# Optimization experiments

Measured on AMD Instinct MI355X. Metric: run time of the kernel, lower is better.

Reference implementation:

```python
import jax, jax.numpy as jnp
import numpy as np

N_REL = 8
N_LAYERS = 2


def setup_inputs() -> dict:
    key = jax.random.key(0)
    ks = jax.random.split(key, 8)
    N, E, D = 32768, 524288, 384
    x = jax.random.normal(ks[0], (N, D), jnp.float32)
    edge_index = jax.random.randint(ks[1], (2, E), 0, N, dtype=jnp.int32)
    edge_type = jax.random.randint(ks[2], (E,), 0, N_REL, dtype=jnp.int32)
    W_rel = jax.random.normal(ks[3], (N_REL, D, D), jnp.float32) * 0.05
    b_rel = jnp.zeros((N_REL, D), jnp.float32)
    norm_constants = jnp.ones((N_REL,), jnp.float32)
    W_mp = jax.random.normal(ks[4], (D, D), jnp.float32) * 0.05
    b_mp = jnp.zeros((D,), jnp.float32)
    W_self = jax.random.normal(ks[5], (D, D), jnp.float32) * 0.05
    b_self = jnp.zeros((D,), jnp.float32)
    return {"x": x, "edge_index": edge_index, "edge_type": edge_type,
            "batch_size": 128, "W_rel": W_rel, "b_rel": b_rel,
            "norm_constants": norm_constants, "W_mp": W_mp, "b_mp": b_mp,
            "W_self": W_self, "b_self": b_self}


def reference(x, edge_index, edge_type, batch_size, W_rel, b_rel,
              norm_constants, W_mp, b_mp, W_self, b_self):
    N = x.shape[0]
    src, dst = edge_index[0], edge_index[1]  # PyG: row0=source j, row1=target i
    # per-edge cosine similarity == pairwise_cosine_similarity(x)[dst, src]
    x_n = x / jnp.linalg.norm(x, axis=1, keepdims=True)
    cos_e = jnp.sum(x_n[dst] * x_n[src], axis=-1)  # [E]
    h = x
    for _ in range(N_LAYERS):
        # ---- RelationAwareMP: per-relation gather-linear-scale-scatter ----
        out = jnp.zeros((N, W_rel.shape[-1]), h.dtype)
        for r in range(N_REL):
            w = jnp.where(edge_type == r, cos_e / norm_constants[r], 0.0)  # [E]
            lin_h = h @ W_rel[r] + b_rel[r]           # [N, D] (linear commutes w/ gather)
            msg = w[:, None] * lin_h[src]             # [E, D]
            out = out + jax.ops.segment_sum(msg, dst, num_segments=N)
        h = jax.nn.relu(out)
        # ---- MP: add-aggregated linear messages + self transform ----
        lin_h = h @ W_mp + b_mp                       # [N, D]
        agg = jax.ops.segment_sum(lin_h[src], dst, num_segments=N)
        h = jax.nn.relu(agg + (h @ W_self + b_self))
    # [N, D] -> [B, N/B, D] -> mean over nodes per graph
    h = h.reshape(batch_size, -1, h.shape[-1])
    return h.mean(axis=1)
```

## Files before the change

kernel.cpp:

```cpp
#include <hip/hip_runtime.h>
#include <stdint.h>

typedef unsigned short u16;
typedef unsigned int u32;
typedef __attribute__((ext_vector_type(4))) float f32x4;
typedef __attribute__((ext_vector_type(8))) short bf16x8;

#define NN 32768
#define EE 524288
#define DD 384
#define NREL 8
#define NGR 128
#define NCAT (NREL * DD)

__device__ __forceinline__ float bf2f(u16 u) {
  union { u32 u; float f; } v; v.u = ((u32)u) << 16; return v.f;
}
__device__ __forceinline__ u16 f2bf(float f) {
  union { float f; u32 u; } v; v.f = f;
  u32 r = v.u + 0x7fffu + ((v.u >> 16) & 1u);
  return (u16)(r >> 16);
}
__device__ __forceinline__ float2 up2(u32 p) {
  return make_float2(bf2f((u16)(p & 0xffffu)), bf2f((u16)(p >> 16)));
}
__device__ __forceinline__ u32 pk2(float a, float b) {
  return (u32)f2bf(a) | ((u32)f2bf(b) << 16);
}
__device__ __forceinline__ void gl16(const u16* g, char* s) {
  __builtin_amdgcn_global_load_lds(
      (const __attribute__((address_space(1))) unsigned int*)(const void*)g,
      (__attribute__((address_space(3))) unsigned int*)(void*)s, 16, 0, 0);
}
__device__ __forceinline__ float dot4(uint4 a, uint4 b) {
  float2 p, q; float acc;
  p = up2(a.x); q = up2(b.x); acc  = p.x * q.x + p.y * q.y;
  p = up2(a.y); q = up2(b.y); acc += p.x * q.x + p.y * q.y;
  p = up2(a.z); q = up2(b.z); acc += p.x * q.x + p.y * q.y;
  p = up2(a.w); q = up2(b.w); acc += p.x * q.x + p.y * q.y;
  return acc;
}

__global__ __launch_bounds__(256) void k_invnorm(const float* __restrict__ x,
                                                 float* __restrict__ invn,
                                                 u16* __restrict__ h0,
                                                 int* __restrict__ cur) {
  const int gid = blockIdx.x * 256 + threadIdx.x;
  if (gid < NN) cur[gid] = 0;
  const int node = gid >> 6;
  const int l = threadIdx.x & 63;
  const float* row = x + (size_t)node * DD;
  float v[6];
  float s = 0.f;
#pragma unroll
  for (int j = 0; j < 6; ++j) { v[j] = row[l + 64 * j]; s += v[j] * v[j]; }
#pragma unroll
  for (int off = 32; off > 0; off >>= 1) s += __shfl_xor(s, off, 64);
  if (l == 0) invn[node] = rsqrtf(s);
  u16* hr = h0 + (size_t)node * DD;
#pragma unroll
  for (int j = 0; j < 6; ++j) hr[l + 64 * j] = f2bf(v[j]);
}

__global__ void k_prepW(const float* __restrict__ Wrel, const float* __restrict__ Wmp,
                        const float* __restrict__ Wself,
                        u16* __restrict__ W3T, u16* __restrict__ W2T) {
  const int i = blockIdx.x * 256 + threadIdx.x;
  const int total1 = NCAT * DD;
  const int total2 = DD * 768;
  if (i < total1) {
    const int ncat = i / DD, k = i % DD;
    const int r = ncat / DD, n = ncat % DD;
    W3T[i] = f2bf(Wrel[(size_t)r * DD * DD + (size_t)k * DD + n]);
  } else if (i < total1 + total2) {
    const int ii = i - total1;
    const int j = ii / 768, k = ii % 768;
    const float v = (k < DD) ? Wmp[k * DD + j] : Wself[(k - DD) * DD + j];
    W2T[ii] = f2bf(v);
  }
}

__global__ __launch_bounds__(256) void k_cos(const u16* __restrict__ H,
                                             const float* __restrict__ invn,
                                             const int* __restrict__ ei,
                                             const int* __restrict__ ety,
                                             const float* __restrict__ ncs,
                                             float* __restrict__ we,
                                             int* __restrict__ cnt) {
  const int e = (int)((blockIdx.x * 256 + threadIdx.x) >> 4);
  const int sub = threadIdx.x & 15;
  const int s = ei[e], d = ei[EE + e];
  const uint4* rs = (const uint4*)(H + (size_t)s * DD);
  const uint4* rd = (const uint4*)(H + (size_t)d * DD);
  float acc = 0.f;
#pragma unroll
  for (int j = 0; j < 3; ++j) acc += dot4(rs[sub + 16 * j], rd[sub + 16 * j]);
#pragma unroll
  for (int m = 1; m < 16; m <<= 1) acc += __shfl_xor(acc, m, 64);
  if (sub == 0) {
    we[e] = acc * invn[s] * invn[d] / ncs[ety[e]];
    atomicAdd(&cnt[d], 1);
  }
}

__global__ __launch_bounds__(1024) void k_scan(const int* __restrict__ deg,
                                               int* __restrict__ rp,
                                               int* __restrict__ cur) {
  __shared__ int ps[1024];
  const int t = threadIdx.x;
  const int base = t * 32;
  int loc[32];
  int tot = 0;
#pragma unroll
  for (int j = 0; j < 32; ++j) { loc[j] = tot; tot += deg[base + j]; }
  ps[t] = tot;
  __syncthreads();
  for (int off = 1; off < 1024; off <<= 1) {
    const int v = (t >= off) ? ps[t - off] : 0;
    __syncthreads();
    ps[t] += v;
    __syncthreads();
  }
  const int myoff = ps[t] - tot;
#pragma unroll
  for (int j = 0; j < 32; ++j) {
    const int val = myoff + loc[j];
    rp[base + j] = val;
    cur[base + j] = val;
  }
  if (t == 1023) rp[NN] = EE;
}

__global__ void k_scatter(const int* __restrict__ ei, const int* __restrict__ etype,
                          const float* __restrict__ we, int* __restrict__ cur,
                          int* __restrict__ epack, float* __restrict__ wsort) {
  const int e = blockIdx.x * 256 + threadIdx.x;
  const int d = ei[EE + e];
  const int pos = atomicAdd(&cur[d], 1);
  epack[pos] = ei[e] | (etype[e] << 16);
  wsort[pos] = we[e];
}

__global__ __launch_bounds__(256) void k_gemm_lin(
    const u16* __restrict__ A, const u16* __restrict__ Bt,
    u16* __restrict__ lin) {
  constexpr int K = DD;
  constexpr int NT = 24;
  __shared__ __align__(16) u16 As[128 * 64];
  __shared__ __align__(16) u16 Bs[128 * 64];
  const int tid = threadIdx.x;
  const int w = tid >> 6, l = tid & 63;
  const int per = gridDim.x >> 3;
  const int rpx = per / NT;
  const int xcd = blockIdx.x & 7;
  const int idx = blockIdx.x >> 3;
  const int mb = (xcd * rpx + idx / NT) * 128;
  const int nb = (idx % NT) * 128;
  const int wr = (w >> 1) * 64;
  const int wc = (w & 1) * 64;
  const int sr = tid >> 3;
  const int swz16 = ((l & 7) ^ (l >> 3)) * 8;
  const int lr = l & 15;
  const int cb = l >> 4;
  const int sx = l & 7;
  char* asb = (char*)As;
  char* bsb = (char*)Bs;
  const int wb = w * 1024;
  f32x4 acc[4][4] = {};
  const u16* a0 = A + (size_t)(mb + sr) * K + swz16;
  const u16* b0 = Bt + (size_t)(nb + sr) * K + swz16;
  const size_t r32 = (size_t)32 * K;
  for (int k0 = 0; k0 < K; k0 += 64) {
    gl16(a0 + k0,           asb + wb);
    gl16(a0 + k0 + r32,     asb + wb + 4096);
    gl16(a0 + k0 + 2 * r32, asb + wb + 8192);
    gl16(a0 + k0 + 3 * r32, asb + wb + 12288);
    gl16(b0 + k0,           bsb + wb);
    gl16(b0 + k0 + r32,     bsb + wb + 4096);
    gl16(b0 + k0 + 2 * r32, bsb + wb + 8192);
    gl16(b0 + k0 + 3 * r32, bsb + wb + 12288);
    __syncthreads();
#pragma unroll
    for (int kk = 0; kk < 64; kk += 32) {
      const int cs = (((kk >> 3) + cb) ^ sx) << 4;
      bf16x8 af[4], bfr[4];
#pragma unroll
      for (int m = 0; m < 4; ++m)
        af[m] = *(const bf16x8*)((const char*)As + (wr + m * 16 + lr) * 128 + cs);
#pragma unroll
      for (int n = 0; n < 4; ++n)
        bfr[n] = *(const bf16x8*)((const char*)Bs + (wc + n * 16 + lr) * 128 + cs);
#pragma unroll
      for (int m = 0; m < 4; ++m)
#pragma unroll
        for (int n = 0; n < 4; ++n)
          acc[m][n] = __builtin_amdgcn_mfma_f32_16x16x32_bf16(af[m], bfr[n], acc[m][n], 0, 0, 0);
    }
    __syncthreads();
  }
  const int lg = l >> 4;
#pragma unroll
  for (int n = 0; n < 4; ++n) {
    const int col = nb + wc + n * 16 + lr;
#pragma unroll
    for (int m = 0; m < 4; ++m) {
#pragma unroll
      for (int q = 0; q < 4; ++q) {
        const int row = mb + wr + m * 16 + lg * 4 + q;
        lin[(size_t)row * NCAT + col] = f2bf(acc[m][n][q]);
      }
    }
  }
}

#define EL_BODY(PK, W)                                                        \
  {                                                                           \
    const int src_ = (PK) & 0xffff;                                           \
    const int ty_ = (PK) >> 16;                                               \
    const u32* r_ = (const u32*)(lin + (size_t)src_ * NCAT + ty_ * DD) + 3 * l; \
    const u32 x0_ = r_[0], x1_ = r_[1], x2_ = r_[2];                          \
    float2 p_;                                                                \
    p_ = up2(x0_); a0 += (W) * p_.x; a1 += (W) * p_.y;                        \
    p_ = up2(x1_); a2 += (W) * p_.x; a3 += (W) * p_.y;                        \
    p_ = up2(x2_); a4 += (W) * p_.x; a5 += (W) * p_.y;                        \
    switch (ty_) {                                                            \
      case 0: s0 += (W); break; case 1: s1 += (W); break;                     \
      case 2: s2 += (W); break; case 3: s3 += (W); break;                     \
      case 4: s4 += (W); break; case 5: s5 += (W); break;                     \
      case 6: s6 += (W); break; default: s7 += (W); break;                    \
    }                                                                         \
  }

__global__ __launch_bounds__(256) void k_edge_lin(
    const u16* __restrict__ lin, const int* __restrict__ rp,
    const int* __restrict__ epack, const float* __restrict__ wsort,
    const float* __restrict__ brel, u16* __restrict__ H2) {
  const int i = blockIdx.x * 4 + (threadIdx.x >> 6);
  const int l = threadIdx.x & 63;
  const int e0 = rp[i], e1 = rp[i + 1];
  float a0 = 0, a1 = 0, a2 = 0, a3 = 0, a4 = 0, a5 = 0;
  float s0 = 0, s1 = 0, s2 = 0, s3 = 0, s4 = 0, s5 = 0, s6 = 0, s7 = 0;
  int e = e0;
  for (; e + 4 <= e1; e += 4) {
    const int pkA = epack[e], pkB = epack[e + 1], pkC = epack[e + 2], pkD = epack[e + 3];
    const float wA = wsort[e], wB = wsort[e + 1], wC = wsort[e + 2], wD = wsort[e + 3];
    EL_BODY(pkA, wA)
    EL_BODY(pkB, wB)
    EL_BODY(pkC, wC)
    EL_BODY(pkD, wD)
  }
  for (; e < e1; ++e) {
    const int pk = epack[e];
    const float w = wsort[e];
    EL_BODY(pk, w)
  }
  const float* bp = brel + 6 * l;
  float b0 = 0, b1 = 0, b2 = 0, b3 = 0, b4 = 0, b5 = 0;
#pragma unroll
  for (int r = 0; r < 8; ++r) {
    const float sr = (r == 0) ? s0 : (r == 1) ? s1 : (r == 2) ? s2 : (r == 3) ? s3
                   : (r == 4) ? s4 : (r == 5) ? s5 : (r == 6) ? s6 : s7;
    const float* bq = bp + r * DD;
    b0 += sr * bq[0]; b1 += sr * bq[1]; b2 += sr * bq[2];
    b3 += sr * bq[3]; b4 += sr * bq[4]; b5 += sr * bq[5];
  }
  u32* o = (u32*)(H2 + (size_t)i * DD + 6 * l);
  o[0] = pk2(fmaxf(a0 + b0, 0.f), fmaxf(a1 + b1, 0.f));
  o[1] = pk2(fmaxf(a2 + b2, 0.f), fmaxf(a3 + b3, 0.f));
  o[2] = pk2(fmaxf(a4 + b4, 0.f), fmaxf(a5 + b5, 0.f));
}

#define ES_BODY(SRC)                                                          \
  {                                                                           \
    const u32* r_ = (const u32*)(H2 + (size_t)(SRC) * DD) + 3 * l;            \
    const u32 x0_ = r_[0], x1_ = r_[1], x2_ = r_[2];                          \
    float2 p_;                                                                \
    p_ = up2(x0_); a0 += p_.x; a1 += p_.y;                                    \
    p_ = up2(x1_); a2 += p_.x; a3 += p_.y;                                    \
    p_ = up2(x2_); a4 += p_.x; a5 += p_.y;                                    \
  }

__global__ __launch_bounds__(256) void k_edge_sum(
    const u16* __restrict__ H2, const int* __restrict__ rp,
    const int* __restrict__ epack, u16* __restrict__ smp) {
  const int i = blockIdx.x * 4 + (threadIdx.x >> 6);
  const int l = threadIdx.x & 63;
  const int e0 = rp[i], e1 = rp[i + 1];
  float a0 = 0, a1 = 0, a2 = 0, a3 = 0, a4 = 0, a5 = 0;
  int e = e0;
  for (; e + 4 <= e1; e += 4) {
    const int sA = epack[e] & 0xffff, sB = epack[e + 1] & 0xffff;
    const int sC = epack[e + 2] & 0xffff, sD = epack[e + 3] & 0xffff;
    ES_BODY(sA) ES_BODY(sB) ES_BODY(sC) ES_BODY(sD)
  }
  for (; e < e1; ++e) {
    const int s = epack[e] & 0xffff;
    ES_BODY(s)
  }
  u32* o = (u32*)(smp + (size_t)i * DD + 6 * l);
  o[0] = pk2(a0, a1);
  o[1] = pk2(a2, a3);
  o[2] = pk2(a4, a5);
}

__global__ __launch_bounds__(256) void k_gemm_mp(
    const u16* __restrict__ A0, const u16* __restrict__ A1,
    const u16* __restrict__ Bt, u16* __restrict__ o_bf,
    const float* __restrict__ bmp, const float* __restrict__ bself,
    const int* __restrict__ rp) {
  constexpr int K = 768;
  constexpr int AS = DD;
  constexpr int NT = 3;
  __shared__ __align__(16) u16 As[128 * 64];
  __shared__ __align__(16) u16 Bs[128 * 64];
  const int tid = threadIdx.x;
  const int w = tid >> 6, l = tid & 63;
  const int per = gridDim.x >> 3;
  const int rpx = per / NT;
  const int xcd = blockIdx.x & 7;
  const int idx = blockIdx.x >> 3;
  const int mb = (xcd * rpx + idx / NT) * 128;
  const int nb = (idx % NT) * 128;
  const int wr = (w >> 1) * 64;
  const int wc = (w & 1) * 64;
  const int sr = tid >> 3;
  const int swz16 = ((l & 7) ^ (l >> 3)) * 8;
  const int lr = l & 15;
  const int cb = l >> 4;
  const int sx = l & 7;
  char* asb = (char*)As;
  char* bsb = (char*)Bs;
  const int wb = w * 1024;
  f32x4 acc[4][4] = {};
  const u16* b0 = Bt + (size_t)(nb + sr) * K + swz16;
  const size_t br32 = (size_t)32 * K;
  const size_t ar32 = (size_t)32 * AS;
  for (int k0 = 0; k0 < K; k0 += 64) {
    const u16* Ab; int ak;
    if (k0 >= DD) { Ab = A1; ak = k0 - DD; }
    else { Ab = A0; ak = k0; }
    const u16* ap = Ab + (size_t)(mb + sr) * AS + ak + swz16;
    gl16(ap,            asb + wb);
    gl16(ap + ar32,     asb + wb + 4096);
    gl16(ap + 2 * ar32, asb + wb + 8192);
    gl16(ap + 3 * ar32, asb + wb + 12288);
    gl16(b0 + k0,            bsb + wb);
    gl16(b0 + k0 + br32,     bsb + wb + 4096);
    gl16(b0 + k0 + 2 * br32, bsb + wb + 8192);
    gl16(b0 + k0 + 3 * br32, bsb + wb + 12288);
    __syncthreads();
#pragma unroll
    for (int kk = 0; kk < 64; kk += 32) {
      const int cs = (((kk >> 3) + cb) ^ sx) << 4;
      bf16x8 af[4], bfr[4];
#pragma unroll
      for (int m = 0; m < 4; ++m)
        af[m] = *(const bf16x8*)((const char*)As + (wr + m * 16 + lr) * 128 + cs);
#pragma unroll
      for (int n = 0; n < 4; ++n)
        bfr[n] = *(const bf16x8*)((const char*)Bs + (wc + n * 16 + lr) * 128 + cs);
#pragma unroll
      for (int m = 0; m < 4; ++m)
#pragma unroll
        for (int n = 0; n < 4; ++n)
          acc[m][n] = __builtin_amdgcn_mfma_f32_16x16x32_bf16(af[m], bfr[n], acc[m][n], 0, 0, 0);
    }
    __syncthreads();
  }
  const int lg = l >> 4;
#pragma unroll
  for (int n = 0; n < 4; ++n) {
    const int col = nb + wc + n * 16 + lr;
    const float bb = bmp[col];
    const float bs = bself[col];
#pragma unroll
    for (int m = 0; m < 4; ++m) {
#pragma unroll
      for (int q = 0; q < 4; ++q) {
        const int row = mb + wr + m * 16 + lg * 4 + q;
        float v = acc[m][n][q];
        const float deg = (float)(rp[row + 1] - rp[row]);
        v = fmaxf(v + deg * bb + bs, 0.f);
        o_bf[(size_t)row * DD + col] = f2bf(v);
      }
    }
  }
}

__global__ __launch_bounds__(192) void k_mean(const u16* __restrict__ H,
                                              float* __restrict__ out) {
  const int g = blockIdx.x, t = threadIdx.x;
  float ax = 0.f, ay = 0.f;
  const u16* base = H + (size_t)g * 256 * DD;
  for (int j = 0; j < 256; ++j) {
    const float2 hv = up2(*(const u32*)(base + (size_t)j * DD + 2 * t));
    ax += hv.x; ay += hv.y;
  }
  out[g * DD + 2 * t]     = ax * (1.f / 256.f);
  out[g * DD + 2 * t + 1] = ay * (1.f / 256.f);
}

extern "C" void kernel_launch(void* const* d_in, const int* in_sizes, int n_in,
                              void* d_out, int out_size, void* d_ws, size_t ws_size,
                              hipStream_t stream) {
  const float* x     = (const float*)d_in[0];
  const int*   ei    = (const int*)d_in[1];
  const int*   ety   = (const int*)d_in[2];
  const float* Wrel  = (const float*)d_in[4];
  const float* brel  = (const float*)d_in[5];
  const float* ncs   = (const float*)d_in[6];
  const float* Wmp   = (const float*)d_in[7];
  const float* bmp   = (const float*)d_in[8];
  const float* Wself = (const float*)d_in[9];
  const float* bself = (const float*)d_in[10];
  float* out = (float*)d_out;
  (void)in_sizes; (void)n_in; (void)out_size; (void)ws_size;

  char* ws = (char*)d_ws;
  size_t off = 0;
  auto alloc = [&](size_t bytes) {
    void* p = ws + off;
    off = (off + bytes + 255) & ~(size_t)255;
    return p;
  };
  float* invn  = (float*)alloc((size_t)NN * 4);
  int*   rp    = (int*)alloc(((size_t)NN + 1) * 4);
  int*   cur   = (int*)alloc((size_t)NN * 4);
  float* we    = (float*)alloc((size_t)EE * 4);
  int*   epack = (int*)alloc((size_t)EE * 4);
  float* wsort = (float*)alloc((size_t)EE * 4);
  u16*   W3T   = (u16*)alloc((size_t)NCAT * DD * 2);
  u16*   W2T   = (u16*)alloc((size_t)DD * 768 * 2);
  u16*   H     = (u16*)alloc((size_t)NN * DD * 2);
  u16*   H2    = (u16*)alloc((size_t)NN * DD * 2);
  u16*   lin   = (u16*)alloc((size_t)NN * NCAT * 2);
  u16*   smp   = lin;

  k_invnorm<<<NN / 4, 256, 0, stream>>>(x, invn, H, cur);
  k_prepW<<<(NCAT * DD + DD * 768 + 255) / 256, 256, 0, stream>>>(Wrel, Wmp, Wself, W3T, W2T);
  k_cos<<<EE / 16, 256, 0, stream>>>(H, invn, ei, ety, ncs, we, cur);
  k_scan<<<1, 1024, 0, stream>>>(cur, rp, cur);
  k_scatter<<<EE / 256, 256, 0, stream>>>(ei, ety, we, cur, epack, wsort);

  for (int layer = 0; layer < 2; ++layer) {
    k_gemm_lin<<<24 * NN / 128, 256, 0, stream>>>(H, W3T, lin);
    k_edge_lin<<<NN / 4, 256, 0, stream>>>(lin, rp, epack, wsort, brel, H2);
    k_edge_sum<<<NN / 4, 256, 0, stream>>>(H2, rp, epack, smp);
    k_gemm_mp<<<3 * NN / 128, 256, 0, stream>>>(smp, H2, W2T, H, bmp, bself, rp);
  }
  k_mean<<<NGR, 192, 0, stream>>>(H, out);
}
```

Measured before the change: 702.8 us.

## Split relation GEMM and edge gather into two halves of four relations

The per-relation linear output (N x 8D bf16, about 200MB) is now computed in two halves of four relations, each followed by an edge-gather pass. The smaller 100MB buffer is meant to fit better in cache (MI355X has a large last-level cache), so the random gathers hit cache more often. The cost is an extra fp32 partial-sum buffer that is written and read back, two more kernel launches, and edge lists that are now scanned twice.

```diff
diff --git a/kernel.cpp b/kernel.cpp
--- a/kernel.cpp
+++ b/kernel.cpp
@@ -12,6 +12,7 @@
 #define NREL 8
 #define NGR 128
 #define NCAT (NREL * DD)
+#define LHALF 1536
 
 __device__ __forceinline__ float bf2f(u16 u) {
   union { u32 u; float f; } v; v.u = ((u32)u) << 16; return v.f;
@@ -142,10 +143,10 @@
 }
 
 __global__ __launch_bounds__(256) void k_gemm_lin(
-    const u16* __restrict__ A, const u16* __restrict__ Bt,
+    const u16* __restrict__ A, const u16* __restrict__ BtH,
     u16* __restrict__ lin) {
   constexpr int K = DD;
-  constexpr int NT = 24;
+  constexpr int NT = 12;
   __shared__ __align__(16) u16 As[128 * 64];
   __shared__ __align__(16) u16 Bs[128 * 64];
   const int tid = threadIdx.x;
@@ -168,7 +169,7 @@
   const int wb = w * 1024;
   f32x4 acc[4][4] = {};
   const u16* a0 = A + (size_t)(mb + sr) * K + swz16;
-  const u16* b0 = Bt + (size_t)(nb + sr) * K + swz16;
+  const u16* b0 = BtH + (size_t)(nb + sr) * K + swz16;
   const size_t r32 = (size_t)32 * K;
   for (int k0 = 0; k0 < K; k0 += 64) {
     gl16(a0 + k0,           asb + wb);
@@ -207,67 +208,80 @@
 #pragma unroll
       for (int q = 0; q < 4; ++q) {
         const int row = mb + wr + m * 16 + lg * 4 + q;
-        lin[(size_t)row * NCAT + col] = f2bf(acc[m][n][q]);
+        lin[(size_t)row * LHALF + col] = f2bf(acc[m][n][q]);
       }
     }
   }
 }
 
-#define EL_BODY(PK, W)                                                        \
+#define EH_BODY(PK, W)                                                        \
   {                                                                           \
-    const int src_ = (PK) & 0xffff;                                           \
     const int ty_ = (PK) >> 16;                                               \
-    const u32* r_ = (const u32*)(lin + (size_t)src_ * NCAT + ty_ * DD) + 3 * l; \
-    const u32 x0_ = r_[0], x1_ = r_[1], x2_ = r_[2];                          \
-    float2 p_;                                                                \
-    p_ = up2(x0_); a0 += (W) * p_.x; a1 += (W) * p_.y;                        \
-    p_ = up2(x1_); a2 += (W) * p_.x; a3 += (W) * p_.y;                        \
-    p_ = up2(x2_); a4 += (W) * p_.x; a5 += (W) * p_.y;                        \
-    switch (ty_) {                                                            \
-      case 0: s0 += (W); break; case 1: s1 += (W); break;                     \
-      case 2: s2 += (W); break; case 3: s3 += (W); break;                     \
-      case 4: s4 += (W); break; case 5: s5 += (W); break;                     \
-      case 6: s6 += (W); break; default: s7 += (W); break;                    \
+    if (PASS == 0 ? (ty_ < 4) : (ty_ >= 4)) {                                 \
+      const int tl_ = PASS == 0 ? ty_ : ty_ - 4;                              \
+      const int src_ = (PK) & 0xffff;                                         \
+      const u32* r_ = (const u32*)(lin + (size_t)src_ * LHALF + tl_ * DD) + 3 * l; \
+      const u32 x0_ = r_[0], x1_ = r_[1], x2_ = r_[2];                        \
+      float2 p_;                                                              \
+      p_ = up2(x0_); a0 += (W) * p_.x; a1 += (W) * p_.y;                      \
+      p_ = up2(x1_); a2 += (W) * p_.x; a3 += (W) * p_.y;                      \
+      p_ = up2(x2_); a4 += (W) * p_.x; a5 += (W) * p_.y;                      \
+      switch (tl_) {                                                          \
+        case 0: s0 += (W); break; case 1: s1 += (W); break;                   \
+        case 2: s2 += (W); break; default: s3 += (W); break;                  \
+      }                                                                       \
     }                                                                         \
   }
 
-__global__ __launch_bounds__(256) void k_edge_lin(
+template <int PASS>
+__global__ __launch_bounds__(256) void k_edge_half(
     const u16* __restrict__ lin, const int* __restrict__ rp,
     const int* __restrict__ epack, const float* __restrict__ wsort,
-    const float* __restrict__ brel, u16* __restrict__ H2) {
+    const float* __restrict__ brel, float* __restrict__ H2acc,
+    u16* __restrict__ H2) {
   const int i = blockIdx.x * 4 + (threadIdx.x >> 6);
   const int l = threadIdx.x & 63;
   const int e0 = rp[i], e1 = rp[i + 1];
   float a0 = 0, a1 = 0, a2 = 0, a3 = 0, a4 = 0, a5 = 0;
-  float s0 = 0, s1 = 0, s2 = 0, s3 = 0, s4 = 0, s5 = 0, s6 = 0, s7 = 0;
+  float s0 = 0, s1 = 0, s2 = 0, s3 = 0;
   int e = e0;
   for (; e + 4 <= e1; e += 4) {
-    const int pkA = epack[e], pkB = epack[e + 1], pkC = epack[e + 2], pkD = epack[e + 3];
-    const float wA = wsort[e], wB = wsort[e + 1], wC = wsort[e + 2], wD = wsort[e + 3];
-    EL_BODY(pkA, wA)
-    EL_BODY(pkB, wB)
-    EL_BODY(pkC, wC)
-    EL_BODY(pkD, wD)
+    int pk[4]; float wv[4];
+#pragma unroll
+    for (int j = 0; j < 4; ++j) { pk[j] = epack[e + j]; wv[j] = wsort[e + j]; }
+#pragma unroll
+    for (int j = 0; j < 4; ++j) EH_BODY(pk[j], wv[j])
   }
   for (; e < e1; ++e) {
     const int pk = epack[e];
     const float w = wsort[e];
-    EL_BODY(pk, w)
-  }
-  const float* bp = brel + 6 * l;
+    EH_BODY(pk, w)
+  }
+  const float* bp = brel + (PASS * 4) * DD + 6 * l;
   float b0 = 0, b1 = 0, b2 = 0, b3 = 0, b4 = 0, b5 = 0;
 #pragma unroll
-  for (int r = 0; r < 8; ++r) {
-    const float sr = (r == 0) ? s0 : (r == 1) ? s1 : (r == 2) ? s2 : (r == 3) ? s3
-                   : (r == 4) ? s4 : (r == 5) ? s5 : (r == 6) ? s6 : s7;
+  for (int r = 0; r < 4; ++r) {
+    const float sr = (r == 0) ? s0 : (r == 1) ? s1 : (r == 2) ? s2 : s3;
     const float* bq = bp + r * DD;
     b0 += sr * bq[0]; b1 += sr * bq[1]; b2 += sr * bq[2];
     b3 += sr * bq[3]; b4 += sr * bq[4]; b5 += sr * bq[5];
   }
-  u32* o = (u32*)(H2 + (size_t)i * DD + 6 * l);
-  o[0] = pk2(fmaxf(a0 + b0, 0.f), fmaxf(a1 + b1, 0.f));
-  o[1] = pk2(fmaxf(a2 + b2, 0.f), fmaxf(a3 + b3, 0.f));
-  o[2] = pk2(fmaxf(a4 + b4, 0.f), fmaxf(a5 + b5, 0.f));
+  float* acc = H2acc + (size_t)i * DD + 6 * l;
+  if (PASS == 0) {
+    acc[0] = a0 + b0; acc[1] = a1 + b1; acc[2] = a2 + b2;
+    acc[3] = a3 + b3; acc[4] = a4 + b4; acc[5] = a5 + b5;
+  } else {
+    const float t0 = fmaxf(acc[0] + a0 + b0, 0.f);
+    const float t1 = fmaxf(acc[1] + a1 + b1, 0.f);
+    const float t2 = fmaxf(acc[2] + a2 + b2, 0.f);
+    const float t3 = fmaxf(acc[3] + a3 + b3, 0.f);
+    const float t4 = fmaxf(acc[4] + a4 + b4, 0.f);
+    const float t5 = fmaxf(acc[5] + a5 + b5, 0.f);
+    u32* o = (u32*)(H2 + (size_t)i * DD + 6 * l);
+    o[0] = pk2(t0, t1);
+    o[1] = pk2(t2, t3);
+    o[2] = pk2(t4, t5);
+  }
 }
 
 #define ES_BODY(SRC)                                                          \
@@ -433,7 +447,8 @@
   u16*   W2T   = (u16*)alloc((size_t)DD * 768 * 2);
   u16*   H     = (u16*)alloc((size_t)NN * DD * 2);
   u16*   H2    = (u16*)alloc((size_t)NN * DD * 2);
-  u16*   lin   = (u16*)alloc((size_t)NN * NCAT * 2);
+  float* H2acc = (float*)alloc((size_t)NN * DD * 4);
+  u16*   lin   = (u16*)alloc((size_t)NN * LHALF * 2);
   u16*   smp   = lin;
 
   k_invnorm<<<NN / 4, 256, 0, stream>>>(x, invn, H, cur);
@@ -443,8 +458,10 @@
   k_scatter<<<EE / 256, 256, 0, stream>>>(ei, ety, we, cur, epack, wsort);
 
   for (int layer = 0; layer < 2; ++layer) {
-    k_gemm_lin<<<24 * NN / 128, 256, 0, stream>>>(H, W3T, lin);
-    k_edge_lin<<<NN / 4, 256, 0, stream>>>(lin, rp, epack, wsort, brel, H2);
+    k_gemm_lin<<<12 * NN / 128, 256, 0, stream>>>(H, W3T, lin);
+    k_edge_half<0><<<NN / 4, 256, 0, stream>>>(lin, rp, epack, wsort, brel, H2acc, nullptr);
+    k_gemm_lin<<<12 * NN / 128, 256, 0, stream>>>(H, W3T + (size_t)LHALF * DD, lin);
+    k_edge_half<1><<<NN / 4, 256, 0, stream>>>(lin, rp, epack, wsort, brel, H2acc, H2);
     k_edge_sum<<<NN / 4, 256, 0, stream>>>(H2, rp, epack, smp);
     k_gemm_mp<<<3 * NN / 128, 256, 0, stream>>>(smp, H2, W2T, H, bmp, bself, rp);
   }
```

Result: slower. 743.1 us (+5.7%).
